# Optimization experiments

Measured on AMD Instinct MI355X. Metric: run time of the kernel, lower is better.

The kernel has to match this reference:

```python
import jax, jax.numpy as jnp
import numpy as np

TAG_SIZE = 64
PAD_TAG, START_TAG, END_TAG = 0, 1, 2
NEG = -10000.0


def setup_inputs() -> dict:
    key = jax.random.key(0)
    kf, kt, kl = jax.random.split(key, 3)
    B, T, K = 2048, 512, TAG_SIZE
    feats = jax.random.normal(kf, (B, T, K), dtype=jnp.float32)
    # transitions init ('randn') with the CRF structural constraints from __init__
    trans = jax.random.normal(kt, (K, K), dtype=jnp.float32)
    trans = trans.at[:, START_TAG].set(NEG)
    trans = trans.at[END_TAG, :].set(NEG)
    trans = trans.at[:, PAD_TAG].set(NEG)
    trans = trans.at[PAD_TAG, :].set(NEG)
    # lengths sorted descending (pack_padded_sequence contract), max length == T
    leng = jax.random.randint(kl, (B,), 1, T + 1, dtype=jnp.int32)
    leng = jnp.sort(leng)[::-1]
    leng = leng.at[0].set(T)
    return {"feats": feats, "leng": leng, "transitions": trans}


def reference(feats, leng, transitions):
    # Faithful padded-form equivalent of CRFLayer.forward -> viterbi_decode.
    B, T, K = feats.shape
    init = jnp.full((B, K), NEG, feats.dtype).at[:, START_TAG].set(0.0)
    end_adj = jnp.where(jnp.arange(K) == END_TAG, 0.0, NEG)  # [K]

    def local_trans(t):
        # local_trans[b,i,j] = transitions[i,j] + feats[b,t,j];
        # at a sentence's last step, subtract 1e4 from all non-END columns.
        lt = transitions[None] + feats[:, t, None, :]  # [B,K,K]
        is_end = (t == leng - 1)[:, None, None]
        return lt + jnp.where(is_end, end_adj[None, None, :], 0.0)

    def step(out, t):
        lt = local_trans(t)                      # [B,K,K]
        scores = lt + out[:, :, None]            # [B,K,K]
        new_out = jnp.max(scores, axis=1)        # [B,K]
        bp = jnp.argmax(scores, axis=1).astype(jnp.int32)
        out = jnp.where((t < leng)[:, None], new_out, out)  # packed: stop updating past leng
        return out, (out, bp)

    _, (out_hist, bp_hist) = jax.lax.scan(step, init, jnp.arange(1, T))
    out_hist = jnp.concatenate([init[None], out_hist], axis=0)                        # [T,B,K]
    bp_hist = jnp.concatenate([jnp.zeros((1, B, K), jnp.int32), bp_hist], axis=0)     # [T,B,K]

    out_end = out_hist[leng - 1, jnp.arange(B)]            # [B,K] score at each sentence end
    tag_scores = jnp.max(out_end, axis=1)                  # [B]
    end_tag = jnp.argmax(out_end, axis=1).astype(jnp.int32)

    # backtrace: tag[leng-1] = end_tag; tag[t] = bp[t+1][tag[t+1]] for t < leng-1; 0 in padding
    bp_next = jnp.concatenate([bp_hist[1:], jnp.zeros((1, B, K), jnp.int32)], axis=0)  # bp_next[t] = bp[t+1]

    def back_step(tag_next, xs):
        t, bp_n = xs
        from_bp = jnp.take_along_axis(bp_n, tag_next[:, None], axis=1)[:, 0]
        tag_t = jnp.where(t == leng - 1, end_tag,
                          jnp.where(t < leng - 1, from_bp, jnp.zeros_like(from_bp)))
        return tag_t, tag_t

    _, tags_rev = jax.lax.scan(back_step, jnp.zeros((B,), jnp.int32),
                               (jnp.arange(T)[::-1], bp_next[::-1]))
    tag_seq = tags_rev[::-1].T                              # [B,T], zero-padded like pad_packed_sequence
    return tag_seq, tag_scores
```

## Files before the change

### kernel.cpp

```cpp
#include <hip/hip_runtime.h>

#define KTAGS 64
#define START_TAG 1
#define END_TAG 2
#define NEGV -10000.0f
#define MAXT 512

__device__ __forceinline__ float rl(float x, int i) {
  return __int_as_float(__builtin_amdgcn_readlane(__float_as_int(x), i));
}

template<bool END>
__device__ __forceinline__ void step64(const float* tc, float feat, float e,
                                       float outj, float& best, int& besti) {
  float gv[8]; int gi[8];
#pragma unroll
  for (int g = 0; g < 8; ++g) {
    float c[8];
#pragma unroll
    for (int k = 0; k < 8; ++k) {
      const int i = g * 8 + k;
      float u = tc[i] + feat;
      if (END) u = u + e;
      c[k] = u + rl(outj, i);
    }
    float va = c[0]; int ia = 0;
    if (c[1] > va) { va = c[1]; ia = 1; }
    float vb = c[2]; int ib = 2;
    if (c[3] > vb) { vb = c[3]; ib = 3; }
    float vc = c[4]; int ic = 4;
    if (c[5] > vc) { vc = c[5]; ic = 5; }
    float vd = c[6]; int id = 6;
    if (c[7] > vd) { vd = c[7]; id = 7; }
    if (vb > va) { va = vb; ia = ib; }
    if (vd > vc) { vc = vd; ic = id; }
    if (vc > va) { va = vc; ia = ic; }
    gv[g] = va; gi[g] = g * 8 + ia;
  }
  if (gv[1] > gv[0]) { gv[0] = gv[1]; gi[0] = gi[1]; }
  if (gv[3] > gv[2]) { gv[2] = gv[3]; gi[2] = gi[3]; }
  if (gv[5] > gv[4]) { gv[4] = gv[5]; gi[4] = gi[5]; }
  if (gv[7] > gv[6]) { gv[6] = gv[7]; gi[6] = gi[7]; }
  if (gv[2] > gv[0]) { gv[0] = gv[2]; gi[0] = gi[2]; }
  if (gv[6] > gv[4]) { gv[4] = gv[6]; gi[4] = gi[6]; }
  if (gv[4] > gv[0]) { gv[0] = gv[4]; gi[0] = gi[4]; }
  best = gv[0]; besti = gi[0];
}

__global__ __launch_bounds__(64) void crf_viterbi(
    const float* __restrict__ feats, const int* __restrict__ leng,
    const float* __restrict__ trans, float* __restrict__ out_tags,
    float* __restrict__ out_scores, int T) {
  const int b = blockIdx.x;
  const int j = threadIdx.x;

  __shared__ unsigned char s_bp[MAXT * KTAGS];
  __shared__ short s_tags[MAXT];

  const int L = leng[b];

  float tc[KTAGS];
#pragma unroll
  for (int i = 0; i < KTAGS; ++i) tc[i] = trans[i * KTAGS + j];

  float outj = (j == START_TAG) ? 0.0f : NEGV;

  const float* fp = feats + (size_t)b * T * KTAGS + j;

  float feat_next = (L > 1) ? fp[1 * KTAGS] : 0.0f;

  for (int t = 1; t < L - 1; ++t) {
    const float feat = feat_next;
    feat_next = fp[(t + 1) * KTAGS];
    float best; int bi;
    step64<false>(tc, feat, 0.0f, outj, best, bi);
    s_bp[t * KTAGS + j] = (unsigned char)bi;
    outj = best;
  }
  if (L > 1) {
    const float e = (j == END_TAG) ? 0.0f : NEGV;
    float best; int bi;
    step64<true>(tc, feat_next, e, outj, best, bi);
    s_bp[(L - 1) * KTAGS + j] = (unsigned char)bi;
    outj = best;
  }

  float v = outj;
  int idx = j;
#pragma unroll
  for (int d = 1; d < 64; d <<= 1) {
    const float ov = __shfl_xor(v, d, 64);
    const int oi = __shfl_xor(idx, d, 64);
    if (ov > v || (ov == v && oi < idx)) { v = ov; idx = oi; }
  }

  __syncthreads();

  int tag = idx;
  if (j == 0) s_tags[L - 1] = (short)tag;
  int row = (L > 1) ? (int)s_bp[(L - 1) * KTAGS + j] : 0;
  for (int t = L - 2; t >= 0; --t) {
    const int row_next = (t > 0) ? (int)s_bp[t * KTAGS + j] : 0;
    tag = __builtin_amdgcn_readlane(row, tag);
    if (j == 0) s_tags[t] = (short)tag;
    row = row_next;
  }
  __syncthreads();

  for (int t = j; t < T; t += 64) {
    out_tags[(size_t)b * T + t] = (t < L) ? (float)s_tags[t] : 0.0f;
  }
  if (j == 0) out_scores[b] = v;
}

extern "C" void kernel_launch(void* const* d_in, const int* in_sizes, int n_in,
                              void* d_out, int out_size, void* d_ws, size_t ws_size,
                              hipStream_t stream) {
  const float* feats = (const float*)d_in[0];
  const int* leng = (const int*)d_in[1];
  const float* trans = (const float*)d_in[2];
  const int B = in_sizes[1];
  const int T = in_sizes[0] / (B * KTAGS);

  float* out_tags = (float*)d_out;
  float* out_scores = out_tags + (size_t)B * T;

  crf_viterbi<<<B, 64, 0, stream>>>(feats, leng, trans, out_tags, out_scores, T);
}
```

Before: 660.4 us.

## Move backpointers from LDS to global workspace to raise occupancy

Adds a kernel variant that stores Viterbi backpointers in a global workspace, packing four bytes per dword, instead of a 32KB shared-memory array. With most LDS freed, more blocks (launch_bounds 64,3) can be resident per CU to hide the serial per-step latency. The backtrace batch-loads eight rows at a time from global memory. In exchange it adds global write and read traffic of B*T*64 bytes, and it falls back to the LDS kernel when the workspace is too small.

New measurement: 781.7 us. 18.4% more time.

```diff
diff --git a/kernel.cpp b/kernel.cpp
--- a/kernel.cpp
+++ b/kernel.cpp
@@ -47,7 +47,88 @@
   best = gv[0]; besti = gi[0];
 }
 
-__global__ __launch_bounds__(64) void crf_viterbi(
+__device__ __forceinline__ void final_argmax(float& v, int& idx) {
+#pragma unroll
+  for (int d = 1; d < 64; d <<= 1) {
+    const float ov = __shfl_xor(v, d, 64);
+    const int oi = __shfl_xor(idx, d, 64);
+    if (ov > v || (ov == v && oi < idx)) { v = ov; idx = oi; }
+  }
+}
+
+__global__ __launch_bounds__(64, 3) void crf_viterbi_ws(
+    const float* __restrict__ feats, const int* __restrict__ leng,
+    const float* __restrict__ trans, float* __restrict__ out_tags,
+    float* __restrict__ out_scores, unsigned char* __restrict__ ws, int T) {
+  const int b = blockIdx.x;
+  const int j = threadIdx.x;
+
+  __shared__ short s_tags[MAXT];
+
+  const int L = leng[b];
+
+  float tc[KTAGS];
+#pragma unroll
+  for (int i = 0; i < KTAGS; ++i) tc[i] = trans[i * KTAGS + j];
+
+  float outj = (j == START_TAG) ? 0.0f : NEGV;
+
+  const float* fp = feats + (size_t)b * T * KTAGS + j;
+  unsigned char* bp = ws + (size_t)b * T * KTAGS;
+  unsigned int* bp32 = (unsigned int*)bp;
+
+  float feat_next = (L > 1) ? fp[1 * KTAGS] : 0.0f;
+  unsigned int pk = 0;
+
+  for (int t = 1; t < L - 1; ++t) {
+    const float feat = feat_next;
+    feat_next = fp[(t + 1) * KTAGS];
+    float best; int bi;
+    step64<false>(tc, feat, 0.0f, outj, best, bi);
+    pk |= ((unsigned)bi) << ((t & 3) * 8);
+    if ((t & 3) == 3) { bp32[(t >> 2) * KTAGS + j] = pk; pk = 0; }
+    outj = best;
+  }
+  if (L > 1) {
+    const int t = L - 1;
+    const float e = (j == END_TAG) ? 0.0f : NEGV;
+    float best; int bi;
+    step64<true>(tc, feat_next, e, outj, best, bi);
+    pk |= ((unsigned)bi) << ((t & 3) * 8);
+    bp32[(t >> 2) * KTAGS + j] = pk;
+    outj = best;
+  }
+
+  float v = outj; int idx = j;
+  final_argmax(v, idx);
+
+  int tag = idx;
+  if (j == 0) s_tags[L - 1] = (short)tag;
+  for (int s_hi = L - 1; s_hi >= 1; s_hi -= 8) {
+    int rowv[8];
+#pragma unroll
+    for (int c = 0; c < 8; ++c) {
+      const int s = s_hi - c;
+      rowv[c] = (s >= 1) ? (int)bp[(s >> 2) * 256 + j * 4 + (s & 3)] : 0;
+    }
+#pragma unroll
+    for (int c = 0; c < 8; ++c) {
+      const int s = s_hi - c;
+      if (s >= 1) {
+        tag = __builtin_amdgcn_readlane(rowv[c], tag);
+        if (j == 0) s_tags[s - 1] = (short)tag;
+      }
+    }
+  }
+  __syncthreads();
+
+  for (int t = j; t < T; t += 64) {
+    out_tags[(size_t)b * T + t] = (t < L) ? (float)s_tags[t] : 0.0f;
+  }
+  if (j == 0) out_scores[b] = v;
+}
+
+__global__ __launch_bounds__(64) void crf_viterbi_lds(
     const float* __restrict__ feats, const int* __restrict__ leng,
     const float* __restrict__ trans, float* __restrict__ out_tags,
     float* __restrict__ out_scores, int T) {
@@ -66,7 +147,6 @@
   float outj = (j == START_TAG) ? 0.0f : NEGV;
 
   const float* fp = feats + (size_t)b * T * KTAGS + j;
-
   float feat_next = (L > 1) ? fp[1 * KTAGS] : 0.0f;
 
   for (int t = 1; t < L - 1; ++t) {
@@ -85,14 +165,8 @@
     outj = best;
   }
 
-  float v = outj;
-  int idx = j;
-#pragma unroll
-  for (int d = 1; d < 64; d <<= 1) {
-    const float ov = __shfl_xor(v, d, 64);
-    const int oi = __shfl_xor(idx, d, 64);
-    if (ov > v || (ov == v && oi < idx)) { v = ov; idx = oi; }
-  }
+  float v = outj; int idx = j;
+  final_argmax(v, idx);
 
   __syncthreads();
 
@@ -125,5 +199,11 @@
   float* out_tags = (float*)d_out;
   float* out_scores = out_tags + (size_t)B * T;
 
-  crf_viterbi<<<B, 64, 0, stream>>>(feats, leng, trans, out_tags, out_scores, T);
-}
+  const size_t need = (size_t)B * T * KTAGS;
+  if (ws_size >= need) {
+    crf_viterbi_ws<<<B, 64, 0, stream>>>(feats, leng, trans, out_tags, out_scores,
+                                         (unsigned char*)d_ws, T);
+  } else {
+    crf_viterbi_lds<<<B, 64, 0, stream>>>(feats, leng, trans, out_tags, out_scores, T);
+  }
+}
```
